# Kernel tuning notes

Hardware: AMD Instinct MI355X
Metric: run time of the kernel (lower is better)

The kernel has to match this reference:

```python
import jax, jax.numpy as jnp
import numpy as np

BETA = 1.0  # init beta


def l2norm(x, eps=1e-12):
    # matches torch F.normalize(dim=-1)
    n = jnp.sqrt(jnp.sum(x * x, axis=-1, keepdims=True))
    return x / jnp.maximum(n, eps)


def setup_inputs() -> dict:
    key = jax.random.key(0)
    k1, k2 = jax.random.split(key)
    B, T, D, N = 8, 2048, 256, 8192
    z = jax.random.normal(k1, (B, T, D), dtype=jnp.float32)
    # EMA codebook weight (buffer, not trained by grad); l2-normalized as the
    # norm-EMA update keeps it on the unit sphere.
    weight = l2norm(jax.random.normal(k2, (N, D), dtype=jnp.float32))
    return {"z": z, "weight": weight}


def reference(z, weight):
    # z: (B, T, D); weight: (N, D)
    z = l2norm(z)
    zf = z.reshape(-1, z.shape[-1])  # (BT, D)
    # squared L2 distances via expansion: |z|^2 + |w|^2 - 2 z.w
    d = (
        jnp.sum(zf * zf, axis=1, keepdims=True)
        + jnp.sum(weight * weight, axis=1)
        - 2.0 * jnp.einsum("bd,nd->bn", zf, weight)
    )  # (BT, N)
    encoding_indices = jnp.argmin(d, axis=1)  # (BT,)
    z_q = weight[encoding_indices].reshape(z.shape)  # (B, T, D)
    # commitment loss: beta * mse(stop_grad(z_q), z)
    loss = BETA * jnp.mean((jax.lax.stop_gradient(z_q) - z) ** 2)
    # straight-through estimator
    z_q = z + jax.lax.stop_gradient(z_q - z)
    encoding_indices = encoding_indices.reshape(z.shape[:-1])  # (B, T)
    return z_q, loss, encoding_indices
```

## Files before the change

kernel.cpp:

```cpp
#include <hip/hip_runtime.h>
#include <float.h>
#include <math.h>


#define BT_ 16384
#define D_  256
#define N_  8192
#define BETA_ 1.0f

#define BM 128
#define BN 256
#define NKT 16
#define NTILES 32

typedef __attribute__((ext_vector_type(8))) _Float16 f16x8;
typedef __attribute__((ext_vector_type(4))) float f32x4;

__device__ __forceinline__ void gld16(void* lds, const void* g) {
  __builtin_amdgcn_global_load_lds(
      (const __attribute__((address_space(1))) void*)g,
      (__attribute__((address_space(3))) void*)lds, 16, 0, 0);
}

__device__ __forceinline__ unsigned short f2h(float x) {
  _Float16 h = (_Float16)x;
  return __builtin_bit_cast(unsigned short, h);
}
__device__ __forceinline__ float h2f(unsigned short u) {
  return (float)__builtin_bit_cast(_Float16, u);
}
__device__ __forceinline__ unsigned ford(float f) {
  unsigned b = __float_as_uint(f);
  return (b & 0x80000000u) ? ~b : (b | 0x80000000u);
}

__global__ __launch_bounds__(256) void k_prep_z(const float* __restrict__ z,
                                                float* __restrict__ zn,
                                                ushort* __restrict__ Acat,
                                                float* __restrict__ rl) {
  const int row  = blockIdx.x * 4 + (threadIdx.x >> 6);
  const int lane = threadIdx.x & 63;
  float4 v = *(reinterpret_cast<const float4*>(z) + (size_t)row * 64 + lane);
  float s = v.x * v.x + v.y * v.y + v.z * v.z + v.w * v.w;
#pragma unroll
  for (int o = 32; o > 0; o >>= 1) s += __shfl_xor(s, o, 64);
  float dn = fmaxf(sqrtf(s), 1e-12f);
  v.x /= dn; v.y /= dn; v.z /= dn; v.w /= dn;
  *(reinterpret_cast<float4*>(zn) + (size_t)row * 64 + lane) = v;
  ushort4 h = make_ushort4(f2h(v.x), f2h(v.y), f2h(v.z), f2h(v.w));
  float lx = v.x - h2f(h.x), ly = v.y - h2f(h.y);
  float lz = v.z - h2f(h.z), lw = v.w - h2f(h.w);
  float s2 = lx * lx + ly * ly + lz * lz + lw * lw;
#pragma unroll
  for (int o = 32; o > 0; o >>= 1) s2 += __shfl_xor(s2, o, 64);
  if (lane == 0) rl[row] = sqrtf(s2);
  ushort4* A4 = reinterpret_cast<ushort4*>(Acat);
  size_t rb = (size_t)row * 128 + lane;
  A4[rb]      = h;
  A4[rb + 64] = h;
}

__global__ __launch_bounds__(256) void k_prep_w(const float* __restrict__ w,
                                                float* __restrict__ wn2,
                                                ushort* __restrict__ Bcat) {
  const int row  = blockIdx.x * 4 + (threadIdx.x >> 6);
  const int lane = threadIdx.x & 63;
  float4 v = *(reinterpret_cast<const float4*>(w) + (size_t)row * 64 + lane);
  float s = v.x * v.x + v.y * v.y + v.z * v.z + v.w * v.w;
#pragma unroll
  for (int o = 32; o > 0; o >>= 1) s += __shfl_xor(s, o, 64);
  if (lane == 0) wn2[row] = s;
  ushort4 h  = make_ushort4(f2h(v.x), f2h(v.y), f2h(v.z), f2h(v.w));
  ushort4 lo = make_ushort4(f2h(v.x - h2f(h.x)), f2h(v.y - h2f(h.y)),
                            f2h(v.z - h2f(h.z)), f2h(v.w - h2f(h.w)));
  ushort4* B4 = reinterpret_cast<ushort4*>(Bcat);
  size_t rb = (size_t)row * 128 + lane;
  B4[rb]      = h;
  B4[rb + 64] = lo;
}

__global__ __launch_bounds__(512, 4) void k_coarse(const ushort* __restrict__ Acat,
                                                   const ushort* __restrict__ Bcat,
                                                   const float* __restrict__ wn2,
                                                   float* __restrict__ tm,
                                                   float* __restrict__ ts,
                                                   int* __restrict__ ti,
                                                   float* __restrict__ tm2) {
  extern __shared__ char smem[];

  const int tid = threadIdx.x;
  const int l   = tid & 63;
  const int wv  = tid >> 6;
  const int wr  = wv >> 2;
  const int wc  = wv & 3;
  const int bid  = blockIdx.x;
  const int xcd  = bid & 7;
  const int q    = bid >> 3;
  const int chnk = q >> 5, wq = q & 31;
  const int rt   = xcd * 16 + (chnk >> 3) * 8 + (wq >> 2);
  const int ct   = (chnk & 7) * 4 + (wq & 3);
  const int row0 = rt * BM;
  const int col0 = ct * BN;

  const int sgr = ((l & 3) ^ ((l >> 3) & 3)) * 16;
  const char* gsrc[3];
  unsigned    ldst[3];
#pragma unroll
  for (int s = 0; s < 3; ++s) {
    int u = wv * 3 + s;
    if (u < 8) {
      gsrc[s] = (const char*)Acat + (size_t)(row0 + u * 16 + (l >> 2)) * 1024 + sgr;
      ldst[s] = u * 1024;
    } else {
      gsrc[s] = (const char*)Bcat + (size_t)(col0 + (u - 8) * 16 + (l >> 2)) * 1024 + sgr;
      ldst[s] = 8192 + (u - 8) * 1024;
    }
  }
#define STAGE(t)                                                               \
  do {                                                                         \
    char* _b = smem + ((t) % 3) * 24576;                                       \
    _Pragma("unroll")                                                          \
    for (int s = 0; s < 3; ++s) gld16(_b + ldst[s], gsrc[s] + (size_t)(t) * 64); \
  } while (0)

  const int lA  = l & 15;
  const int gsw = (lA >> 1) & 3;
  const int gk  = (l >> 4) ^ gsw;
  const unsigned aOff = (unsigned)((wr * 64 + lA) * 64 + gk * 16);
  const unsigned bOff = (unsigned)(8192 + (wc * 64 + lA) * 64 + gk * 16);

  f32x4 acc[4][4];
#pragma unroll
  for (int i = 0; i < 4; ++i)
#pragma unroll
    for (int j = 0; j < 4; ++j) acc[i][j] = (f32x4){0.f, 0.f, 0.f, 0.f};

  STAGE(0);
  STAGE(1);

  for (int t = 0; t < NKT; ++t) {
    char* buf = smem + (t % 3) * 24576;
    if (t < NKT - 1) asm volatile("s_waitcnt vmcnt(3)" ::: "memory");
    else             asm volatile("s_waitcnt vmcnt(0)" ::: "memory");
    __builtin_amdgcn_s_barrier();
    __builtin_amdgcn_sched_barrier(0);
    if (t + 2 < NKT) STAGE(t + 2);

    f16x8 af[4], bg[4];
#pragma unroll
    for (int i = 0; i < 4; ++i)
      af[i] = *(const f16x8*)(buf + aOff + i * 1024);
#pragma unroll
    for (int j = 0; j < 4; ++j)
      bg[j] = *(const f16x8*)(buf + bOff + j * 1024);
    __builtin_amdgcn_s_setprio(1);
#pragma unroll
    for (int i = 0; i < 4; ++i)
#pragma unroll
      for (int j = 0; j < 4; ++j)
        acc[i][j] = __builtin_amdgcn_mfma_f32_16x16x32_f16(af[i], bg[j], acc[i][j], 0, 0, 0);
    __builtin_amdgcn_s_setprio(0);
  }
#undef STAGE

  float wnv[4];
#pragma unroll
  for (int n = 0; n < 4; ++n) wnv[n] = wn2[col0 + wc * 64 + n * 16 + lA];
  float* pm = (float*)smem;
  float* ps = (float*)(smem + 16896);
  int*   pc = (int*)(smem + 33792);
  __syncthreads();

#pragma unroll
  for (int i = 0; i < 4; ++i) {
#pragma unroll
    for (int qq = 0; qq < 4; ++qq) {
      float m = FLT_MAX, s = FLT_MAX; int c = 0;
#pragma unroll
      for (int j = 0; j < 4; ++j) {
        float d = fmaf(-2.0f, acc[i][j][qq], wnv[j]);
        int cc = wc * 64 + j * 16 + lA;
        if (d < m) { s = m; m = d; c = cc; }
        else if (d < s) s = d;
      }
      float om = __shfl_xor(m, 8, 64);
      float os = __shfl_xor(s, 8, 64);
      int   oc = __shfl_xor(c, 8, 64);
      float ns = fminf(fminf(s, os), fmaxf(m, om));
      if (om < m || (om == m && oc < c)) { m = om; c = oc; }
      s = ns;
      if ((l & 8) == 0) {
        int row = wr * 64 + i * 16 + (l >> 4) * 4 + qq;
        int w33 = row * 33 + wc * 8 + (l & 7);
        pm[w33] = m; ps[w33] = s; pc[w33] = c;
      }
    }
  }
  __syncthreads();
  {
    const int row = tid >> 2;
    const int qd  = tid & 3;
    float gm = FLT_MAX, gs = FLT_MAX; int gc = 0x7fffffff;
#pragma unroll
    for (int k = 0; k < 8; ++k) {
      int w33 = row * 33 + qd * 8 + k;
      float m = pm[w33], s = ps[w33]; int c = pc[w33];
      float ns = fminf(fminf(gs, s), fmaxf(gm, m));
      if (m < gm || (m == gm && c < gc)) { gm = m; gc = c; }
      gs = ns;
    }
    tm2[(size_t)(row0 + row) * 128 + ct * 4 + qd] = gm;
#pragma unroll
    for (int msk = 1; msk <= 2; msk <<= 1) {
      float om = __shfl_xor(gm, msk, 64);
      float os = __shfl_xor(gs, msk, 64);
      int   oc = __shfl_xor(gc, msk, 64);
      float ns = fminf(fminf(gs, os), fmaxf(gm, om));
      if (om < gm || (om == gm && oc < gc)) { gm = om; gc = oc; }
      gs = ns;
    }
    if (qd == 0) {
      size_t o = (size_t)ct * BT_ + row0 + row;
      tm[o] = gm; ts[o] = gs; ti[o] = col0 + gc;
    }
  }
}

__global__ __launch_bounds__(256) void k_combine(const float* __restrict__ tm,
                                                 const float* __restrict__ ts,
                                                 const int* __restrict__ ti,
                                                 const float* __restrict__ rl,
                                                 int* __restrict__ idxf,
                                                 float* __restrict__ lim,
                                                 unsigned long long* __restrict__ rowKey,
                                                 int* __restrict__ flagged,
                                                 int* __restrict__ count) {
  const int row = blockIdx.x * 256 + threadIdx.x;
  float m = FLT_MAX, s = FLT_MAX; int bi = 0x7fffffff;
#pragma unroll
  for (int t = 0; t < NTILES; ++t) {
    size_t o = (size_t)t * BT_ + row;
    float om = tm[o], os = ts[o]; int oi = ti[o];
    float nsv = fminf(fminf(s, os), fmaxf(m, om));
    if (om < m || (om == m && oi < bi)) { m = om; bi = oi; }
    s = nsv;
  }
  idxf[row] = bi;
  const float thr = 4.0f * rl[row] + 2.5e-4f;
  if (s - m <= thr) {
    rowKey[row] = ~0ULL;
    lim[row] = m + thr;
    int p = atomicAdd(count, 1);
    flagged[p] = row;
  } else {
    rowKey[row] = 0ULL;
  }
}

__global__ __launch_bounds__(256) void k_refine(const float* __restrict__ zn,
                                                const float* __restrict__ w,
                                                const float* __restrict__ wn2,
                                                const float* __restrict__ tm2,
                                                const float* __restrict__ lim,
                                                const int* __restrict__ flagged,
                                                const int* __restrict__ count,
                                                unsigned long long* __restrict__ rowKey) {
  __shared__ float4 znr[64];
  __shared__ int cand[128];
  __shared__ int ncand;
  const int tid = threadIdx.x;
  const int l   = tid & 63;
  const int wv  = tid >> 6;
  const int cnt = *count;
  for (int f = blockIdx.x; f < cnt; f += gridDim.x) {
    __syncthreads();
    const int row = flagged[f];
    if (tid == 0) ncand = 0;
    if (tid < 64)
      znr[tid] = *(reinterpret_cast<const float4*>(zn) + (size_t)row * 64 + tid);
    __syncthreads();
    const float lv = lim[row];
    if (tid < 128) {
      float t2 = tm2[(size_t)row * 128 + tid];
      if (t2 <= lv) { int p = atomicAdd(&ncand, 1); cand[p] = tid; }
    }
    __syncthreads();
    const int nc = ncand;
    unsigned long long key = ~0ULL;
    for (int i = wv; i < nc; i += 4) {
      const int g = cand[i];
      const int c = g * 64 + l;
      const float4* wr4 = reinterpret_cast<const float4*>(w) + (size_t)c * 64;
      float d0 = 0.f, d1 = 0.f, d2 = 0.f, d3 = 0.f;
#pragma unroll
      for (int k4 = 0; k4 < 16; ++k4) {
        float4 a0 = znr[k4 * 4 + 0], b0 = wr4[k4 * 4 + 0];
        float4 a1 = znr[k4 * 4 + 1], b1 = wr4[k4 * 4 + 1];
        float4 a2 = znr[k4 * 4 + 2], b2 = wr4[k4 * 4 + 2];
        float4 a3 = znr[k4 * 4 + 3], b3 = wr4[k4 * 4 + 3];
        d0 = fmaf(a0.x, b0.x, d0); d0 = fmaf(a0.y, b0.y, d0);
        d0 = fmaf(a0.z, b0.z, d0); d0 = fmaf(a0.w, b0.w, d0);
        d1 = fmaf(a1.x, b1.x, d1); d1 = fmaf(a1.y, b1.y, d1);
        d1 = fmaf(a1.z, b1.z, d1); d1 = fmaf(a1.w, b1.w, d1);
        d2 = fmaf(a2.x, b2.x, d2); d2 = fmaf(a2.y, b2.y, d2);
        d2 = fmaf(a2.z, b2.z, d2); d2 = fmaf(a2.w, b2.w, d2);
        d3 = fmaf(a3.x, b3.x, d3); d3 = fmaf(a3.y, b3.y, d3);
        d3 = fmaf(a3.z, b3.z, d3); d3 = fmaf(a3.w, b3.w, d3);
      }
      float dot = (d0 + d1) + (d2 + d3);
      float d = fmaf(-2.0f, dot, wn2[c]);
      unsigned long long k = ((unsigned long long)ford(d) << 32) | (unsigned)c;
      key = (k < key) ? k : key;
    }
#pragma unroll
    for (int msk = 1; msk < 64; msk <<= 1) {
      unsigned long long ok = __shfl_xor(key, msk, 64);
      key = (ok < key) ? ok : key;
    }
    if (l == 0 && key != ~0ULL) atomicMin(&rowKey[row], key);
  }
}

__global__ __launch_bounds__(256) void k_gather(const float* __restrict__ zn,
                                                const float* __restrict__ w,
                                                const int* __restrict__ idxf,
                                                const unsigned long long* __restrict__ rowKey,
                                                float* __restrict__ zq,
                                                float* __restrict__ idx_out,
                                                float* __restrict__ wpart) {
  const int row  = blockIdx.x * 4 + (threadIdx.x >> 6);
  const int lane = threadIdx.x & 63;
  unsigned long long key = rowKey[row];
  const int bi = (key == 0ULL) ? idxf[row] : (int)(key & 0xFFFFFFFFu);
  float4 cv = *(reinterpret_cast<const float4*>(w)  + (size_t)bi  * 64 + lane);
  float4 zv = *(reinterpret_cast<const float4*>(zn) + (size_t)row * 64 + lane);
  *(reinterpret_cast<float4*>(zq) + (size_t)row * 64 + lane) = cv;
  float dx = cv.x - zv.x, dy = cv.y - zv.y, dz = cv.z - zv.z, dw = cv.w - zv.w;
  float s = dx * dx + dy * dy + dz * dz + dw * dw;
#pragma unroll
  for (int o = 32; o > 0; o >>= 1) s += __shfl_xor(s, o, 64);
  if (lane == 0) {
    wpart[row] = s;
    idx_out[row] = (float)bi;
  }
}

__global__ __launch_bounds__(256) void k_final(const float* __restrict__ wpart,
                                               float* __restrict__ loss_out) {
  __shared__ float wsum[4];
  float s = 0.f;
  for (int i = threadIdx.x; i < BT_; i += 256) s += wpart[i];
#pragma unroll
  for (int o = 32; o > 0; o >>= 1) s += __shfl_xor(s, o, 64);
  if ((threadIdx.x & 63) == 0) wsum[threadIdx.x >> 6] = s;
  __syncthreads();
  if (threadIdx.x == 0)
    loss_out[0] = BETA_ * ((wsum[0] + wsum[1]) + (wsum[2] + wsum[3])) *
                  (1.0f / (float)(BT_ * D_));
}

extern "C" void kernel_launch(void* const* d_in, const int* in_sizes, int n_in,
                              void* d_out, int out_size, void* d_ws, size_t ws_size,
                              hipStream_t stream) {
  const float* z = (const float*)d_in[0];
  const float* w = (const float*)d_in[1];

  float* out      = (float*)d_out;
  float* zq       = out;
  float* loss_out = out + (size_t)BT_ * D_;
  float* idx_out  = loss_out + 1;

  char* wsb = (char*)d_ws;
  float*  zn      = (float*)(wsb);
  ushort* Acat    = (ushort*)(wsb + 16777216);
  ushort* Bcat    = (ushort*)(wsb + 33554432);
  float*  tm      = (float*)(wsb + 41943040);
  float*  ts      = (float*)(wsb + 46137344);
  int*    ti      = (int*)(wsb + 50331648);
  float*  tm2     = (float*)(wsb + 54525952);
  float*  wn2     = (float*)(wsb + 62914560);
  float*  rl      = (float*)(wsb + 62947328);
  int*    idxf    = (int*)(wsb + 63012864);
  float*  lim     = (float*)(wsb + 63078400);
  unsigned long long* rowKey = (unsigned long long*)(wsb + 63143936);
  int*    flagged = (int*)(wsb + 63275008);
  int*    count   = (int*)(wsb + 63340544);
  float*  wpart   = ts;

  hipFuncSetAttribute((const void*)k_coarse,
                      hipFuncAttributeMaxDynamicSharedMemorySize, 73728);

  hipMemsetAsync(count, 0, 4, stream);
  k_prep_z<<<BT_ / 4, 256, 0, stream>>>(z, zn, Acat, rl);
  k_prep_w<<<N_ / 4, 256, 0, stream>>>(w, wn2, Bcat);
  k_coarse<<<(BT_ / BM) * NTILES, 512, 73728, stream>>>(Acat, Bcat, wn2, tm, ts, ti, tm2);
  k_combine<<<BT_ / 256, 256, 0, stream>>>(tm, ts, ti, rl, idxf, lim, rowKey, flagged, count);
  k_refine<<<2048, 256, 0, stream>>>(zn, w, wn2, tm2, lim, flagged, count, rowKey);
  k_gather<<<BT_ / 4, 256, 0, stream>>>(zn, w, idxf, rowKey, zq, idx_out, wpart);
  k_final<<<1, 256, 0, stream>>>(wpart, loss_out);
}
```

Baseline: 247.5 us.

## Stop duplicating z in fp16 GEMM, load A from registers, merge prep kernels

Acat previously held the fp16 z twice so that a single GEMM over K=512 could multiply it against the hi and lo halves of the codebook. Now Acat holds one copy, and each A fragment is loaded straight from global memory into registers. That fragment is reused across two MFMA passes, one against the hi part and one against the lo part of B staged in LDS. This halves A traffic and the prep writes, and cuts the LDS pipeline from three to two stages. The two prep kernels are fused into one launch. The trade-off is that global A loads are no longer staged through LDS and the pipeline is shallower, which may expose more latency.

```diff
diff --git a/kernel.cpp b/kernel.cpp
--- a/kernel.cpp
+++ b/kernel.cpp
@@ -10,7 +10,7 @@
 
 #define BM 128
 #define BN 256
-#define NKT 16
+#define NKT 8
 #define NTILES 32
 
 typedef __attribute__((ext_vector_type(8))) _Float16 f16x8;
@@ -34,49 +34,47 @@
   return (b & 0x80000000u) ? ~b : (b | 0x80000000u);
 }
 
-__global__ __launch_bounds__(256) void k_prep_z(const float* __restrict__ z,
-                                                float* __restrict__ zn,
-                                                ushort* __restrict__ Acat,
-                                                float* __restrict__ rl) {
-  const int row  = blockIdx.x * 4 + (threadIdx.x >> 6);
+__global__ __launch_bounds__(256) void k_prep(const float* __restrict__ z,
+                                              const float* __restrict__ w,
+                                              float* __restrict__ zn,
+                                              ushort* __restrict__ Acat,
+                                              float* __restrict__ rl,
+                                              float* __restrict__ wn2,
+                                              ushort* __restrict__ Bcat) {
+  const int b    = blockIdx.x;
   const int lane = threadIdx.x & 63;
-  float4 v = *(reinterpret_cast<const float4*>(z) + (size_t)row * 64 + lane);
-  float s = v.x * v.x + v.y * v.y + v.z * v.z + v.w * v.w;
-#pragma unroll
-  for (int o = 32; o > 0; o >>= 1) s += __shfl_xor(s, o, 64);
-  float dn = fmaxf(sqrtf(s), 1e-12f);
-  v.x /= dn; v.y /= dn; v.z /= dn; v.w /= dn;
-  *(reinterpret_cast<float4*>(zn) + (size_t)row * 64 + lane) = v;
-  ushort4 h = make_ushort4(f2h(v.x), f2h(v.y), f2h(v.z), f2h(v.w));
-  float lx = v.x - h2f(h.x), ly = v.y - h2f(h.y);
-  float lz = v.z - h2f(h.z), lw = v.w - h2f(h.w);
-  float s2 = lx * lx + ly * ly + lz * lz + lw * lw;
-#pragma unroll
-  for (int o = 32; o > 0; o >>= 1) s2 += __shfl_xor(s2, o, 64);
-  if (lane == 0) rl[row] = sqrtf(s2);
-  ushort4* A4 = reinterpret_cast<ushort4*>(Acat);
-  size_t rb = (size_t)row * 128 + lane;
-  A4[rb]      = h;
-  A4[rb + 64] = h;
-}
-
-__global__ __launch_bounds__(256) void k_prep_w(const float* __restrict__ w,
-                                                float* __restrict__ wn2,
-                                                ushort* __restrict__ Bcat) {
-  const int row  = blockIdx.x * 4 + (threadIdx.x >> 6);
-  const int lane = threadIdx.x & 63;
-  float4 v = *(reinterpret_cast<const float4*>(w) + (size_t)row * 64 + lane);
-  float s = v.x * v.x + v.y * v.y + v.z * v.z + v.w * v.w;
-#pragma unroll
-  for (int o = 32; o > 0; o >>= 1) s += __shfl_xor(s, o, 64);
-  if (lane == 0) wn2[row] = s;
-  ushort4 h  = make_ushort4(f2h(v.x), f2h(v.y), f2h(v.z), f2h(v.w));
-  ushort4 lo = make_ushort4(f2h(v.x - h2f(h.x)), f2h(v.y - h2f(h.y)),
-                            f2h(v.z - h2f(h.z)), f2h(v.w - h2f(h.w)));
-  ushort4* B4 = reinterpret_cast<ushort4*>(Bcat);
-  size_t rb = (size_t)row * 128 + lane;
-  B4[rb]      = h;
-  B4[rb + 64] = lo;
+  if (b < BT_ / 4) {
+    const int row = b * 4 + (threadIdx.x >> 6);
+    float4 v = *(reinterpret_cast<const float4*>(z) + (size_t)row * 64 + lane);
+    float s = v.x * v.x + v.y * v.y + v.z * v.z + v.w * v.w;
+#pragma unroll
+    for (int o = 32; o > 0; o >>= 1) s += __shfl_xor(s, o, 64);
+    float dn = fmaxf(sqrtf(s), 1e-12f);
+    v.x /= dn; v.y /= dn; v.z /= dn; v.w /= dn;
+    *(reinterpret_cast<float4*>(zn) + (size_t)row * 64 + lane) = v;
+    ushort4 h = make_ushort4(f2h(v.x), f2h(v.y), f2h(v.z), f2h(v.w));
+    float lx = v.x - h2f(h.x), ly = v.y - h2f(h.y);
+    float lz = v.z - h2f(h.z), lw = v.w - h2f(h.w);
+    float s2 = lx * lx + ly * ly + lz * lz + lw * lw;
+#pragma unroll
+    for (int o = 32; o > 0; o >>= 1) s2 += __shfl_xor(s2, o, 64);
+    if (lane == 0) rl[row] = sqrtf(s2);
+    reinterpret_cast<ushort4*>(Acat)[(size_t)row * 64 + lane] = h;
+  } else {
+    const int row = (b - BT_ / 4) * 4 + (threadIdx.x >> 6);
+    float4 v = *(reinterpret_cast<const float4*>(w) + (size_t)row * 64 + lane);
+    float s = v.x * v.x + v.y * v.y + v.z * v.z + v.w * v.w;
+#pragma unroll
+    for (int o = 32; o > 0; o >>= 1) s += __shfl_xor(s, o, 64);
+    if (lane == 0) wn2[row] = s;
+    ushort4 h  = make_ushort4(f2h(v.x), f2h(v.y), f2h(v.z), f2h(v.w));
+    ushort4 lo = make_ushort4(f2h(v.x - h2f(h.x)), f2h(v.y - h2f(h.y)),
+                              f2h(v.z - h2f(h.z)), f2h(v.w - h2f(h.w)));
+    ushort4* B4 = reinterpret_cast<ushort4*>(Bcat);
+    size_t rb = (size_t)row * 128 + lane;
+    B4[rb]      = h;
+    B4[rb + 64] = lo;
+  }
 }
 
 __global__ __launch_bounds__(512, 4) void k_coarse(const ushort* __restrict__ Acat,
@@ -103,31 +101,33 @@
   const int col0 = ct * BN;
 
   const int sgr = ((l & 3) ^ ((l >> 3) & 3)) * 16;
-  const char* gsrc[3];
-  unsigned    ldst[3];
-#pragma unroll
-  for (int s = 0; s < 3; ++s) {
-    int u = wv * 3 + s;
-    if (u < 8) {
-      gsrc[s] = (const char*)Acat + (size_t)(row0 + u * 16 + (l >> 2)) * 1024 + sgr;
-      ldst[s] = u * 1024;
-    } else {
-      gsrc[s] = (const char*)Bcat + (size_t)(col0 + (u - 8) * 16 + (l >> 2)) * 1024 + sgr;
-      ldst[s] = 8192 + (u - 8) * 1024;
-    }
+  const char* gsrc[4];
+  unsigned    ldst[4];
+#pragma unroll
+  for (int s = 0; s < 4; ++s) {
+    int u = wv * 4 + s;
+    gsrc[s] = (const char*)Bcat + (size_t)(col0 + (u & 15) * 16 + (l >> 2)) * 1024 +
+              (u >> 4) * 512 + sgr;
+    ldst[s] = u * 1024;
   }
 #define STAGE(t)                                                               \
   do {                                                                         \
-    char* _b = smem + ((t) % 3) * 24576;                                       \
+    char* _b = smem + ((t) & 1) * 32768;                                       \
     _Pragma("unroll")                                                          \
-    for (int s = 0; s < 3; ++s) gld16(_b + ldst[s], gsrc[s] + (size_t)(t) * 64); \
+    for (int s = 0; s < 4; ++s) gld16(_b + ldst[s], gsrc[s] + (size_t)(t) * 64); \
   } while (0)
 
-  const int lA  = l & 15;
-  const int gsw = (lA >> 1) & 3;
-  const int gk  = (l >> 4) ^ gsw;
-  const unsigned aOff = (unsigned)((wr * 64 + lA) * 64 + gk * 16);
-  const unsigned bOff = (unsigned)(8192 + (wc * 64 + lA) * 64 + gk * 16);
+  const int lA = l & 15;
+  const ushort* aB = Acat + (size_t)(row0 + wr * 64 + lA) * 256 + (l >> 4) * 8;
+#define LOADA(t)                                                               \
+  do {                                                                         \
+    _Pragma("unroll")                                                          \
+    for (int i = 0; i < 4; ++i)                                                \
+      af[i] = *(const f16x8*)(aB + i * 4096 + (t) * 32);                       \
+  } while (0)
+
+  const int gk = (l >> 4) ^ ((lA >> 1) & 3);
+  const unsigned bOff = (unsigned)((wc * 64 + lA) * 64 + gk * 16);
 
   f32x4 acc[4][4];
 #pragma unroll
@@ -135,21 +135,19 @@
 #pragma unroll
     for (int j = 0; j < 4; ++j) acc[i][j] = (f32x4){0.f, 0.f, 0.f, 0.f};
 
+  f16x8 af[4];
   STAGE(0);
-  STAGE(1);
-
+  LOADA(0);
+
+#pragma unroll
   for (int t = 0; t < NKT; ++t) {
-    char* buf = smem + (t % 3) * 24576;
-    if (t < NKT - 1) asm volatile("s_waitcnt vmcnt(3)" ::: "memory");
-    else             asm volatile("s_waitcnt vmcnt(0)" ::: "memory");
+    char* buf = smem + (t & 1) * 32768;
+    asm volatile("s_waitcnt vmcnt(0)" ::: "memory");
     __builtin_amdgcn_s_barrier();
     __builtin_amdgcn_sched_barrier(0);
-    if (t + 2 < NKT) STAGE(t + 2);
-
-    f16x8 af[4], bg[4];
-#pragma unroll
-    for (int i = 0; i < 4; ++i)
-      af[i] = *(const f16x8*)(buf + aOff + i * 1024);
+    if (t + 1 < NKT) STAGE(t + 1);
+
+    f16x8 bg[4];
 #pragma unroll
     for (int j = 0; j < 4; ++j)
       bg[j] = *(const f16x8*)(buf + bOff + j * 1024);
@@ -160,8 +158,20 @@
       for (int j = 0; j < 4; ++j)
         acc[i][j] = __builtin_amdgcn_mfma_f32_16x16x32_f16(af[i], bg[j], acc[i][j], 0, 0, 0);
     __builtin_amdgcn_s_setprio(0);
+#pragma unroll
+    for (int j = 0; j < 4; ++j)
+      bg[j] = *(const f16x8*)(buf + 16384 + bOff + j * 1024);
+    __builtin_amdgcn_s_setprio(1);
+#pragma unroll
+    for (int i = 0; i < 4; ++i)
+#pragma unroll
+      for (int j = 0; j < 4; ++j)
+        acc[i][j] = __builtin_amdgcn_mfma_f32_16x16x32_f16(af[i], bg[j], acc[i][j], 0, 0, 0);
+    __builtin_amdgcn_s_setprio(0);
+    if (t + 1 < NKT) LOADA(t + 1);
   }
 #undef STAGE
+#undef LOADA
 
   float wnv[4];
 #pragma unroll
@@ -373,27 +383,26 @@
   char* wsb = (char*)d_ws;
   float*  zn      = (float*)(wsb);
   ushort* Acat    = (ushort*)(wsb + 16777216);
-  ushort* Bcat    = (ushort*)(wsb + 33554432);
-  float*  tm      = (float*)(wsb + 41943040);
-  float*  ts      = (float*)(wsb + 46137344);
-  int*    ti      = (int*)(wsb + 50331648);
-  float*  tm2     = (float*)(wsb + 54525952);
-  float*  wn2     = (float*)(wsb + 62914560);
-  float*  rl      = (float*)(wsb + 62947328);
-  int*    idxf    = (int*)(wsb + 63012864);
-  float*  lim     = (float*)(wsb + 63078400);
-  unsigned long long* rowKey = (unsigned long long*)(wsb + 63143936);
-  int*    flagged = (int*)(wsb + 63275008);
-  int*    count   = (int*)(wsb + 63340544);
+  ushort* Bcat    = (ushort*)(wsb + 25165824);
+  float*  tm      = (float*)(wsb + 33554432);
+  float*  ts      = (float*)(wsb + 37748736);
+  int*    ti      = (int*)(wsb + 41943040);
+  float*  tm2     = (float*)(wsb + 46137344);
+  float*  wn2     = (float*)(wsb + 54525952);
+  float*  rl      = (float*)(wsb + 54558720);
+  int*    idxf    = (int*)(wsb + 54624256);
+  float*  lim     = (float*)(wsb + 54689792);
+  unsigned long long* rowKey = (unsigned long long*)(wsb + 54755328);
+  int*    flagged = (int*)(wsb + 54886400);
+  int*    count   = (int*)(wsb + 54951936);
   float*  wpart   = ts;
 
   hipFuncSetAttribute((const void*)k_coarse,
-                      hipFuncAttributeMaxDynamicSharedMemorySize, 73728);
+                      hipFuncAttributeMaxDynamicSharedMemorySize, 65536);
 
   hipMemsetAsync(count, 0, 4, stream);
-  k_prep_z<<<BT_ / 4, 256, 0, stream>>>(z, zn, Acat, rl);
-  k_prep_w<<<N_ / 4, 256, 0, stream>>>(w, wn2, Bcat);
-  k_coarse<<<(BT_ / BM) * NTILES, 512, 73728, stream>>>(Acat, Bcat, wn2, tm, ts, ti, tm2);
+  k_prep<<<BT_ / 4 + N_ / 4, 256, 0, stream>>>(z, w, zn, Acat, rl, wn2, Bcat);
+  k_coarse<<<(BT_ / BM) * NTILES, 512, 65536, stream>>>(Acat, Bcat, wn2, tm, ts, ti, tm2);
   k_combine<<<BT_ / 256, 256, 0, stream>>>(tm, ts, ti, rl, idxf, lim, rowKey, flagged, count);
   k_refine<<<2048, 256, 0, stream>>>(zn, w, wn2, tm2, lim, flagged, count, rowKey);
   k_gather<<<BT_ / 4, 256, 0, stream>>>(zn, w, idxf, rowKey, zq, idx_out, wpart);
```

Result: slower. 293.5 us (+18.6%).

## Drop split-fp16 residual terms from coarse GEMM and widen refine threshold

Applied to the files above, without the earlier changes.

The coarse distance GEMM previously used concatenated hi/lo fp16 operands (K doubled to 512) to approximate fp32 dot products. It now uses only the fp16 high part (K=256), which halves the MFMA work and operand traffic in k_coarse. To stay exact, the candidate threshold now adds the maximum codebook rounding residual, computed with an atomicMax, so more rows may be flagged for fp32 refinement. The two prep kernels are also merged into one launch, and fp16 subnormals are flushed to zero.

```diff
diff --git a/kernel.cpp b/kernel.cpp
--- a/kernel.cpp
+++ b/kernel.cpp
@@ -10,7 +10,7 @@
 
 #define BM 128
 #define BN 256
-#define NKT 16
+#define NKT 8
 #define NTILES 32
 
 typedef __attribute__((ext_vector_type(8))) _Float16 f16x8;
@@ -23,6 +23,7 @@
 }
 
 __device__ __forceinline__ unsigned short f2h(float x) {
+  if (fabsf(x) < 6.103515625e-5f) return 0;
   _Float16 h = (_Float16)x;
   return __builtin_bit_cast(unsigned short, h);
 }
@@ -34,49 +35,49 @@
   return (b & 0x80000000u) ? ~b : (b | 0x80000000u);
 }
 
-__global__ __launch_bounds__(256) void k_prep_z(const float* __restrict__ z,
-                                                float* __restrict__ zn,
-                                                ushort* __restrict__ Acat,
-                                                float* __restrict__ rl) {
-  const int row  = blockIdx.x * 4 + (threadIdx.x >> 6);
+__global__ __launch_bounds__(256) void k_prep(const float* __restrict__ z,
+                                              const float* __restrict__ w,
+                                              float* __restrict__ zn,
+                                              ushort* __restrict__ Acat,
+                                              float* __restrict__ rl,
+                                              float* __restrict__ wn2,
+                                              ushort* __restrict__ Bcat,
+                                              int* __restrict__ wlmax) {
+  const int b    = blockIdx.x;
   const int lane = threadIdx.x & 63;
-  float4 v = *(reinterpret_cast<const float4*>(z) + (size_t)row * 64 + lane);
-  float s = v.x * v.x + v.y * v.y + v.z * v.z + v.w * v.w;
-#pragma unroll
-  for (int o = 32; o > 0; o >>= 1) s += __shfl_xor(s, o, 64);
-  float dn = fmaxf(sqrtf(s), 1e-12f);
-  v.x /= dn; v.y /= dn; v.z /= dn; v.w /= dn;
-  *(reinterpret_cast<float4*>(zn) + (size_t)row * 64 + lane) = v;
-  ushort4 h = make_ushort4(f2h(v.x), f2h(v.y), f2h(v.z), f2h(v.w));
-  float lx = v.x - h2f(h.x), ly = v.y - h2f(h.y);
-  float lz = v.z - h2f(h.z), lw = v.w - h2f(h.w);
-  float s2 = lx * lx + ly * ly + lz * lz + lw * lw;
-#pragma unroll
-  for (int o = 32; o > 0; o >>= 1) s2 += __shfl_xor(s2, o, 64);
-  if (lane == 0) rl[row] = sqrtf(s2);
-  ushort4* A4 = reinterpret_cast<ushort4*>(Acat);
-  size_t rb = (size_t)row * 128 + lane;
-  A4[rb]      = h;
-  A4[rb + 64] = h;
-}
-
-__global__ __launch_bounds__(256) void k_prep_w(const float* __restrict__ w,
-                                                float* __restrict__ wn2,
-                                                ushort* __restrict__ Bcat) {
-  const int row  = blockIdx.x * 4 + (threadIdx.x >> 6);
-  const int lane = threadIdx.x & 63;
-  float4 v = *(reinterpret_cast<const float4*>(w) + (size_t)row * 64 + lane);
-  float s = v.x * v.x + v.y * v.y + v.z * v.z + v.w * v.w;
-#pragma unroll
-  for (int o = 32; o > 0; o >>= 1) s += __shfl_xor(s, o, 64);
-  if (lane == 0) wn2[row] = s;
-  ushort4 h  = make_ushort4(f2h(v.x), f2h(v.y), f2h(v.z), f2h(v.w));
-  ushort4 lo = make_ushort4(f2h(v.x - h2f(h.x)), f2h(v.y - h2f(h.y)),
-                            f2h(v.z - h2f(h.z)), f2h(v.w - h2f(h.w)));
-  ushort4* B4 = reinterpret_cast<ushort4*>(Bcat);
-  size_t rb = (size_t)row * 128 + lane;
-  B4[rb]      = h;
-  B4[rb + 64] = lo;
+  if (b < BT_ / 4) {
+    const int row = b * 4 + (threadIdx.x >> 6);
+    float4 v = *(reinterpret_cast<const float4*>(z) + (size_t)row * 64 + lane);
+    float s = v.x * v.x + v.y * v.y + v.z * v.z + v.w * v.w;
+#pragma unroll
+    for (int o = 32; o > 0; o >>= 1) s += __shfl_xor(s, o, 64);
+    float dn = fmaxf(sqrtf(s), 1e-12f);
+    v.x /= dn; v.y /= dn; v.z /= dn; v.w /= dn;
+    *(reinterpret_cast<float4*>(zn) + (size_t)row * 64 + lane) = v;
+    ushort4 h = make_ushort4(f2h(v.x), f2h(v.y), f2h(v.z), f2h(v.w));
+    float lx = v.x - h2f(h.x), ly = v.y - h2f(h.y);
+    float lz = v.z - h2f(h.z), lw = v.w - h2f(h.w);
+    float s2 = lx * lx + ly * ly + lz * lz + lw * lw;
+#pragma unroll
+    for (int o = 32; o > 0; o >>= 1) s2 += __shfl_xor(s2, o, 64);
+    if (lane == 0) rl[row] = sqrtf(s2);
+    reinterpret_cast<ushort4*>(Acat)[(size_t)row * 64 + lane] = h;
+  } else {
+    const int row = (b - BT_ / 4) * 4 + (threadIdx.x >> 6);
+    float4 v = *(reinterpret_cast<const float4*>(w) + (size_t)row * 64 + lane);
+    float s = v.x * v.x + v.y * v.y + v.z * v.z + v.w * v.w;
+#pragma unroll
+    for (int o = 32; o > 0; o >>= 1) s += __shfl_xor(s, o, 64);
+    if (lane == 0) wn2[row] = s;
+    ushort4 h = make_ushort4(f2h(v.x), f2h(v.y), f2h(v.z), f2h(v.w));
+    float lx = v.x - h2f(h.x), ly = v.y - h2f(h.y);
+    float lz = v.z - h2f(h.z), lw = v.w - h2f(h.w);
+    float s2 = lx * lx + ly * ly + lz * lz + lw * lw;
+#pragma unroll
+    for (int o = 32; o > 0; o >>= 1) s2 += __shfl_xor(s2, o, 64);
+    if (lane == 0) atomicMax(wlmax, __float_as_int(sqrtf(s2)));
+    reinterpret_cast<ushort4*>(Bcat)[(size_t)row * 64 + lane] = h;
+  }
 }
 
 __global__ __launch_bounds__(512, 4) void k_coarse(const ushort* __restrict__ Acat,
@@ -109,10 +110,10 @@
   for (int s = 0; s < 3; ++s) {
     int u = wv * 3 + s;
     if (u < 8) {
-      gsrc[s] = (const char*)Acat + (size_t)(row0 + u * 16 + (l >> 2)) * 1024 + sgr;
+      gsrc[s] = (const char*)Acat + (size_t)(row0 + u * 16 + (l >> 2)) * 512 + sgr;
       ldst[s] = u * 1024;
     } else {
-      gsrc[s] = (const char*)Bcat + (size_t)(col0 + (u - 8) * 16 + (l >> 2)) * 1024 + sgr;
+      gsrc[s] = (const char*)Bcat + (size_t)(col0 + (u - 8) * 16 + (l >> 2)) * 512 + sgr;
       ldst[s] = 8192 + (u - 8) * 1024;
     }
   }
@@ -124,8 +125,7 @@
   } while (0)
 
   const int lA  = l & 15;
-  const int gsw = (lA >> 1) & 3;
-  const int gk  = (l >> 4) ^ gsw;
+  const int gk  = (l >> 4) ^ ((lA >> 1) & 3);
   const unsigned aOff = (unsigned)((wr * 64 + lA) * 64 + gk * 16);
   const unsigned bOff = (unsigned)(8192 + (wc * 64 + lA) * 64 + gk * 16);
 
@@ -230,6 +230,7 @@
                                                  const float* __restrict__ ts,
                                                  const int* __restrict__ ti,
                                                  const float* __restrict__ rl,
+                                                 const int* __restrict__ wlmax,
                                                  int* __restrict__ idxf,
                                                  float* __restrict__ lim,
                                                  unsigned long long* __restrict__ rowKey,
@@ -246,7 +247,8 @@
     s = nsv;
   }
   idxf[row] = bi;
-  const float thr = 4.0f * rl[row] + 2.5e-4f;
+  const float wlm = __int_as_float(*wlmax);
+  const float thr = 4.0f * (rl[row] + wlm) + 2.5e-4f;
   if (s - m <= thr) {
     rowKey[row] = ~0ULL;
     lim[row] = m + thr;
@@ -373,28 +375,28 @@
   char* wsb = (char*)d_ws;
   float*  zn      = (float*)(wsb);
   ushort* Acat    = (ushort*)(wsb + 16777216);
-  ushort* Bcat    = (ushort*)(wsb + 33554432);
-  float*  tm      = (float*)(wsb + 41943040);
-  float*  ts      = (float*)(wsb + 46137344);
-  int*    ti      = (int*)(wsb + 50331648);
-  float*  tm2     = (float*)(wsb + 54525952);
-  float*  wn2     = (float*)(wsb + 62914560);
-  float*  rl      = (float*)(wsb + 62947328);
-  int*    idxf    = (int*)(wsb + 63012864);
-  float*  lim     = (float*)(wsb + 63078400);
-  unsigned long long* rowKey = (unsigned long long*)(wsb + 63143936);
-  int*    flagged = (int*)(wsb + 63275008);
-  int*    count   = (int*)(wsb + 63340544);
+  ushort* Bcat    = (ushort*)(wsb + 25165824);
+  float*  tm      = (float*)(wsb + 29360128);
+  float*  ts      = (float*)(wsb + 31457280);
+  int*    ti      = (int*)(wsb + 33554432);
+  float*  tm2     = (float*)(wsb + 35651584);
+  float*  wn2     = (float*)(wsb + 44040192);
+  float*  rl      = (float*)(wsb + 44072960);
+  int*    idxf    = (int*)(wsb + 44138496);
+  float*  lim     = (float*)(wsb + 44204032);
+  unsigned long long* rowKey = (unsigned long long*)(wsb + 44269568);
+  int*    flagged = (int*)(wsb + 44400640);
+  int*    count   = (int*)(wsb + 44466176);
+  int*    wlmax   = (int*)(wsb + 44466180);
   float*  wpart   = ts;
 
   hipFuncSetAttribute((const void*)k_coarse,
                       hipFuncAttributeMaxDynamicSharedMemorySize, 73728);
 
-  hipMemsetAsync(count, 0, 4, stream);
-  k_prep_z<<<BT_ / 4, 256, 0, stream>>>(z, zn, Acat, rl);
-  k_prep_w<<<N_ / 4, 256, 0, stream>>>(w, wn2, Bcat);
+  hipMemsetAsync(count, 0, 8, stream);
+  k_prep<<<BT_ / 4 + N_ / 4, 256, 0, stream>>>(z, w, zn, Acat, rl, wn2, Bcat, wlmax);
   k_coarse<<<(BT_ / BM) * NTILES, 512, 73728, stream>>>(Acat, Bcat, wn2, tm, ts, ti, tm2);
-  k_combine<<<BT_ / 256, 256, 0, stream>>>(tm, ts, ti, rl, idxf, lim, rowKey, flagged, count);
+  k_combine<<<BT_ / 256, 256, 0, stream>>>(tm, ts, ti, rl, wlmax, idxf, lim, rowKey, flagged, count);
   k_refine<<<2048, 256, 0, stream>>>(zn, w, wn2, tm2, lim, flagged, count, rowKey);
   k_gather<<<BT_ / 4, 256, 0, stream>>>(zn, w, idxf, rowKey, zq, idx_out, wpart);
   k_final<<<1, 256, 0, stream>>>(wpart, loss_out);
```

Result: slower. 300.7 us (+21.5%).

## Double-buffer coarse GEMM to cut LDS and merge prep kernels into one launch

Applied to the files above, without the earlier changes.

The coarse GEMM's cp.async-style LDS pipeline drops from three buffers to two, with a full vmcnt(0) wait each iteration. This cuts dynamic LDS from 72KB to 48KB so more workgroups can be resident per CU. The epilogue stores candidate column indices as ushort so the reduction scratch still fits in the smaller allocation. The z and w preparation kernels are merged into one launch with branch-by-block, removing one launch. The risk is that the shallower prefetch depth exposes more global-load latency per K step.

```diff
diff --git a/kernel.cpp b/kernel.cpp
--- a/kernel.cpp
+++ b/kernel.cpp
@@ -34,49 +34,50 @@
   return (b & 0x80000000u) ? ~b : (b | 0x80000000u);
 }
 
-__global__ __launch_bounds__(256) void k_prep_z(const float* __restrict__ z,
-                                                float* __restrict__ zn,
-                                                ushort* __restrict__ Acat,
-                                                float* __restrict__ rl) {
-  const int row  = blockIdx.x * 4 + (threadIdx.x >> 6);
+__global__ __launch_bounds__(256) void k_prep(const float* __restrict__ z,
+                                              const float* __restrict__ w,
+                                              float* __restrict__ zn,
+                                              ushort* __restrict__ Acat,
+                                              float* __restrict__ rl,
+                                              float* __restrict__ wn2,
+                                              ushort* __restrict__ Bcat) {
+  const int b    = blockIdx.x;
   const int lane = threadIdx.x & 63;
-  float4 v = *(reinterpret_cast<const float4*>(z) + (size_t)row * 64 + lane);
-  float s = v.x * v.x + v.y * v.y + v.z * v.z + v.w * v.w;
-#pragma unroll
-  for (int o = 32; o > 0; o >>= 1) s += __shfl_xor(s, o, 64);
-  float dn = fmaxf(sqrtf(s), 1e-12f);
-  v.x /= dn; v.y /= dn; v.z /= dn; v.w /= dn;
-  *(reinterpret_cast<float4*>(zn) + (size_t)row * 64 + lane) = v;
-  ushort4 h = make_ushort4(f2h(v.x), f2h(v.y), f2h(v.z), f2h(v.w));
-  float lx = v.x - h2f(h.x), ly = v.y - h2f(h.y);
-  float lz = v.z - h2f(h.z), lw = v.w - h2f(h.w);
-  float s2 = lx * lx + ly * ly + lz * lz + lw * lw;
-#pragma unroll
-  for (int o = 32; o > 0; o >>= 1) s2 += __shfl_xor(s2, o, 64);
-  if (lane == 0) rl[row] = sqrtf(s2);
-  ushort4* A4 = reinterpret_cast<ushort4*>(Acat);
-  size_t rb = (size_t)row * 128 + lane;
-  A4[rb]      = h;
-  A4[rb + 64] = h;
-}
-
-__global__ __launch_bounds__(256) void k_prep_w(const float* __restrict__ w,
-                                                float* __restrict__ wn2,
-                                                ushort* __restrict__ Bcat) {
-  const int row  = blockIdx.x * 4 + (threadIdx.x >> 6);
-  const int lane = threadIdx.x & 63;
-  float4 v = *(reinterpret_cast<const float4*>(w) + (size_t)row * 64 + lane);
-  float s = v.x * v.x + v.y * v.y + v.z * v.z + v.w * v.w;
-#pragma unroll
-  for (int o = 32; o > 0; o >>= 1) s += __shfl_xor(s, o, 64);
-  if (lane == 0) wn2[row] = s;
-  ushort4 h  = make_ushort4(f2h(v.x), f2h(v.y), f2h(v.z), f2h(v.w));
-  ushort4 lo = make_ushort4(f2h(v.x - h2f(h.x)), f2h(v.y - h2f(h.y)),
-                            f2h(v.z - h2f(h.z)), f2h(v.w - h2f(h.w)));
-  ushort4* B4 = reinterpret_cast<ushort4*>(Bcat);
-  size_t rb = (size_t)row * 128 + lane;
-  B4[rb]      = h;
-  B4[rb + 64] = lo;
+  if (b < BT_ / 4) {
+    const int row = b * 4 + (threadIdx.x >> 6);
+    float4 v = *(reinterpret_cast<const float4*>(z) + (size_t)row * 64 + lane);
+    float s = v.x * v.x + v.y * v.y + v.z * v.z + v.w * v.w;
+#pragma unroll
+    for (int o = 32; o > 0; o >>= 1) s += __shfl_xor(s, o, 64);
+    float dn = fmaxf(sqrtf(s), 1e-12f);
+    v.x /= dn; v.y /= dn; v.z /= dn; v.w /= dn;
+    *(reinterpret_cast<float4*>(zn) + (size_t)row * 64 + lane) = v;
+    ushort4 h = make_ushort4(f2h(v.x), f2h(v.y), f2h(v.z), f2h(v.w));
+    float lx = v.x - h2f(h.x), ly = v.y - h2f(h.y);
+    float lz = v.z - h2f(h.z), lw = v.w - h2f(h.w);
+    float s2 = lx * lx + ly * ly + lz * lz + lw * lw;
+#pragma unroll
+    for (int o = 32; o > 0; o >>= 1) s2 += __shfl_xor(s2, o, 64);
+    if (lane == 0) rl[row] = sqrtf(s2);
+    ushort4* A4 = reinterpret_cast<ushort4*>(Acat);
+    size_t rb = (size_t)row * 128 + lane;
+    A4[rb]      = h;
+    A4[rb + 64] = h;
+  } else {
+    const int row = (b - BT_ / 4) * 4 + (threadIdx.x >> 6);
+    float4 v = *(reinterpret_cast<const float4*>(w) + (size_t)row * 64 + lane);
+    float s = v.x * v.x + v.y * v.y + v.z * v.z + v.w * v.w;
+#pragma unroll
+    for (int o = 32; o > 0; o >>= 1) s += __shfl_xor(s, o, 64);
+    if (lane == 0) wn2[row] = s;
+    ushort4 h  = make_ushort4(f2h(v.x), f2h(v.y), f2h(v.z), f2h(v.w));
+    ushort4 lo = make_ushort4(f2h(v.x - h2f(h.x)), f2h(v.y - h2f(h.y)),
+                              f2h(v.z - h2f(h.z)), f2h(v.w - h2f(h.w)));
+    ushort4* B4 = reinterpret_cast<ushort4*>(Bcat);
+    size_t rb = (size_t)row * 128 + lane;
+    B4[rb]      = h;
+    B4[rb + 64] = lo;
+  }
 }
 
 __global__ __launch_bounds__(512, 4) void k_coarse(const ushort* __restrict__ Acat,
@@ -118,14 +119,13 @@
   }
 #define STAGE(t)                                                               \
   do {                                                                         \
-    char* _b = smem + ((t) % 3) * 24576;                                       \
+    char* _b = smem + ((t) & 1) * 24576;                                       \
     _Pragma("unroll")                                                          \
     for (int s = 0; s < 3; ++s) gld16(_b + ldst[s], gsrc[s] + (size_t)(t) * 64); \
   } while (0)
 
   const int lA  = l & 15;
-  const int gsw = (lA >> 1) & 3;
-  const int gk  = (l >> 4) ^ gsw;
+  const int gk  = (l >> 4) ^ ((lA >> 1) & 3);
   const unsigned aOff = (unsigned)((wr * 64 + lA) * 64 + gk * 16);
   const unsigned bOff = (unsigned)(8192 + (wc * 64 + lA) * 64 + gk * 16);
 
@@ -136,15 +136,13 @@
     for (int j = 0; j < 4; ++j) acc[i][j] = (f32x4){0.f, 0.f, 0.f, 0.f};
 
   STAGE(0);
-  STAGE(1);
 
   for (int t = 0; t < NKT; ++t) {
-    char* buf = smem + (t % 3) * 24576;
-    if (t < NKT - 1) asm volatile("s_waitcnt vmcnt(3)" ::: "memory");
-    else             asm volatile("s_waitcnt vmcnt(0)" ::: "memory");
+    char* buf = smem + (t & 1) * 24576;
+    asm volatile("s_waitcnt vmcnt(0)" ::: "memory");
     __builtin_amdgcn_s_barrier();
     __builtin_amdgcn_sched_barrier(0);
-    if (t + 2 < NKT) STAGE(t + 2);
+    if (t + 1 < NKT) STAGE(t + 1);
 
     f16x8 af[4], bg[4];
 #pragma unroll
@@ -166,9 +164,9 @@
   float wnv[4];
 #pragma unroll
   for (int n = 0; n < 4; ++n) wnv[n] = wn2[col0 + wc * 64 + n * 16 + lA];
-  float* pm = (float*)smem;
-  float* ps = (float*)(smem + 16896);
-  int*   pc = (int*)(smem + 33792);
+  float*  pm = (float*)smem;
+  float*  ps = (float*)(smem + 16896);
+  ushort* pc = (ushort*)(smem + 33792);
   __syncthreads();
 
 #pragma unroll
@@ -192,7 +190,7 @@
       if ((l & 8) == 0) {
         int row = wr * 64 + i * 16 + (l >> 4) * 4 + qq;
         int w33 = row * 33 + wc * 8 + (l & 7);
-        pm[w33] = m; ps[w33] = s; pc[w33] = c;
+        pm[w33] = m; ps[w33] = s; pc[w33] = (ushort)c;
       }
     }
   }
@@ -204,7 +202,7 @@
 #pragma unroll
     for (int k = 0; k < 8; ++k) {
       int w33 = row * 33 + qd * 8 + k;
-      float m = pm[w33], s = ps[w33]; int c = pc[w33];
+      float m = pm[w33], s = ps[w33]; int c = (int)pc[w33];
       float ns = fminf(fminf(gs, s), fmaxf(gm, m));
       if (m < gm || (m == gm && c < gc)) { gm = m; gc = c; }
       gs = ns;
@@ -388,12 +386,11 @@
   float*  wpart   = ts;
 
   hipFuncSetAttribute((const void*)k_coarse,
-                      hipFuncAttributeMaxDynamicSharedMemorySize, 73728);
+                      hipFuncAttributeMaxDynamicSharedMemorySize, 49152);
 
   hipMemsetAsync(count, 0, 4, stream);
-  k_prep_z<<<BT_ / 4, 256, 0, stream>>>(z, zn, Acat, rl);
-  k_prep_w<<<N_ / 4, 256, 0, stream>>>(w, wn2, Bcat);
-  k_coarse<<<(BT_ / BM) * NTILES, 512, 73728, stream>>>(Acat, Bcat, wn2, tm, ts, ti, tm2);
+  k_prep<<<BT_ / 4 + N_ / 4, 256, 0, stream>>>(z, w, zn, Acat, rl, wn2, Bcat);
+  k_coarse<<<(BT_ / BM) * NTILES, 512, 49152, stream>>>(Acat, Bcat, wn2, tm, ts, ti, tm2);
   k_combine<<<BT_ / 256, 256, 0, stream>>>(tm, ts, ti, rl, idxf, lim, rowKey, flagged, count);
   k_refine<<<2048, 256, 0, stream>>>(zn, w, wn2, tm2, lim, flagged, count, rowKey);
   k_gather<<<BT_ / 4, 256, 0, stream>>>(zn, w, idxf, rowKey, zq, idx_out, wpart);
```

New measurement: 254.6 us. 2.9% more time.
